# Performance work log

Measured on AMD Instinct MI355X. Metric: run time of the kernel, lower is better.

## Reference

```python
import jax, jax.numpy as jnp
import numpy as np
import math


def setup_inputs() -> dict:
    key = jax.random.key(0)
    ks = jax.random.split(key, 8)
    B, C, H, W = 8, 512, 48, 48
    Cq = C // 8
    s = 0.05
    return {
        "x": jax.random.normal(ks[0], (B, C, H, W), jnp.float32),
        "Wq": jax.random.normal(ks[1], (Cq, C), jnp.float32) * s,
        "bq": jax.random.normal(ks[2], (Cq,), jnp.float32) * s,
        "Wk": jax.random.normal(ks[3], (Cq, C), jnp.float32) * s,
        "bk": jax.random.normal(ks[4], (Cq,), jnp.float32) * s,
        "Wv": jax.random.normal(ks[5], (C, C), jnp.float32) * s,
        "bv": jax.random.normal(ks[6], (C,), jnp.float32) * s,
        "gamma": jax.random.normal(ks[7], (1,), jnp.float32),
    }


def reference(x, Wq, bq, Wk, bk, Wv, bv, gamma):
    B, C, H, W = x.shape
    Cq = Wq.shape[0]
    N = H * W
    xf = x.reshape(B, C, N)  # 1x1 conv == channel matmul
    q = jnp.einsum('oc,bcn->bno', Wq, xf) + bq  # [B, N, Cq] (proj_query, permuted)
    k = jnp.einsum('oc,bcn->bon', Wk, xf) + bk[None, :, None]  # [B, Cq, N]
    v = jnp.einsum('oc,bcn->bon', Wv, xf) + bv[None, :, None]  # [B, C, N]
    # ave_I = (1/Cq)*(I - (1/Cq)*J); Q @ ave_I = (Q - rowmean(Q)) / Cq
    qc = (q - jnp.mean(q, axis=-1, keepdims=True)) / Cq
    sigma = jnp.einsum('bnc,bcm->bnm', qc, k) / math.sqrt(Cq)  # [B, N, N]
    attention = jax.nn.softmax(sigma, axis=-1)
    # out = V @ attention^T : out[b,c,n] = sum_m v[b,c,m] * attention[b,n,m]
    am = jnp.einsum('bcm,bnm->bcn', v, attention).reshape(B, C, H, W)
    out = gamma[0] * am + x
    return out
```

## Files before the change

kernel.cpp:

```cpp
#include <hip/hip_runtime.h>

#define B_ 8
#define C_ 512
#define N_ 2304
#define CQ 64

typedef float f32x2 __attribute__((ext_vector_type(2)));
typedef float f32x4 __attribute__((ext_vector_type(4)));
typedef float f32x16 __attribute__((ext_vector_type(16)));
typedef short bf16x8 __attribute__((ext_vector_type(8)));
typedef unsigned short u16x4 __attribute__((ext_vector_type(4)));
typedef unsigned short u16x8 __attribute__((ext_vector_type(8)));
typedef int i32x2 __attribute__((ext_vector_type(2)));
typedef int i32x4 __attribute__((ext_vector_type(4)));

__device__ __forceinline__ unsigned short f2bf(float f){
  union { float f; unsigned int u; } v; v.f = f;
  unsigned int r = (v.u + 0x7fffu + ((v.u >> 16) & 1u)) >> 16;
  return (unsigned short)r;
}

__device__ __forceinline__ void gload_lds16(const void* g, void* l){
  __builtin_amdgcn_global_load_lds(
      (const __attribute__((address_space(1))) unsigned int*)g,
      (__attribute__((address_space(3))) unsigned int*)l, 16, 0, 0);
}

__global__ __launch_bounds__(256) void k_wcvt(const float* __restrict__ Wq,
                                              const float* __restrict__ Wk,
                                              const float* __restrict__ Wv,
                                              unsigned short* __restrict__ Wb){
  int idx = blockIdx.x*256 + threadIdx.x;
  int h = idx & 1, ln = (idx >> 1) & 31, cs = (idx >> 6) & 31, ob = idx >> 11;
  int row = ob*32 + ln, col = cs*16 + h*8;
  const float* src;
  if (row < 64)       src = Wq + (size_t)row*512 + col;
  else if (row < 128) src = Wk + (size_t)(row-64)*512 + col;
  else                src = Wv + (size_t)(row-128)*512 + col;
  f32x4 v0 = *(const f32x4*)src;
  f32x4 v1 = *(const f32x4*)(src + 4);
  u16x8 o;
  #pragma unroll
  for (int j = 0; j < 4; j++){ o[j] = f2bf(v0[j]); o[4+j] = f2bf(v1[j]); }
  *(u16x8*)(Wb + (size_t)idx*8) = o;
}

__global__ __launch_bounds__(512) void k_prep(const float* __restrict__ x,
                                              const float* __restrict__ bq,
                                              const float* __restrict__ bk,
                                              const float* __restrict__ bv,
                                              const unsigned short* __restrict__ Wb,
                                              unsigned short* __restrict__ qw,
                                              unsigned short* __restrict__ kw,
                                              unsigned char* __restrict__ vw8){
  __shared__ short xt_l[32*520];
  __shared__ float scr[2*32*68];

  int i = blockIdx.x; int b = i & 7; int nt = i >> 3;
  int n0 = nt*32;
  int t = threadIdx.x; int w = t >> 6; int l = t & 63;
  int h = l >> 5, ln = l & 31;
  const size_t bN = (size_t)b*N_;

  #pragma unroll
  for (int it = 0; it < 8; it++){
    int c = it*64 + (t >> 3);
    int n4 = (t & 7)*4;
    f32x4 v = *(const f32x4*)(x + ((size_t)b*C_ + c)*N_ + n0 + n4);
    #pragma unroll
    for (int j = 0; j < 4; j++) xt_l[(n4+j)*520 + c] = (short)f2bf(v[j]);
  }
  __syncthreads();

  const unsigned short* wlane = Wb + (size_t)(ln*2 + h)*8;
  const unsigned short* wv0 = wlane + (size_t)(4 + 2*w)*16384;
  const unsigned short* wv1 = wlane + (size_t)(5 + 2*w)*16384;
  const unsigned short* wqk = wlane + (size_t)w*16384;

  f32x16 vacc[2]; f32x16 qkacc;
  #pragma unroll
  for (int rr = 0; rr < 16; rr++){ vacc[0][rr]=0.f; vacc[1][rr]=0.f; qkacc[rr]=0.f; }

  #pragma unroll 8
  for (int cs = 0; cs < 32; cs++){
    bf16x8 bx = *(const bf16x8*)&xt_l[ln*520 + cs*16 + h*8];
    bf16x8 a0 = *(const bf16x8*)(wv0 + (size_t)cs*512);
    bf16x8 a1 = *(const bf16x8*)(wv1 + (size_t)cs*512);
    vacc[0] = __builtin_amdgcn_mfma_f32_32x32x16_bf16(a0, bx, vacc[0], 0, 0, 0);
    vacc[1] = __builtin_amdgcn_mfma_f32_32x32x16_bf16(a1, bx, vacc[1], 0, 0, 0);
    if (w < 4){
      bf16x8 aq = *(const bf16x8*)(wqk + (size_t)cs*512);
      qkacc = __builtin_amdgcn_mfma_f32_32x32x16_bf16(aq, bx, qkacc, 0, 0, 0);
    }
  }

  if (w < 4){
    float* s = scr + ((w >> 1) ? 2176 : 0);
    int obase = (w & 1)*32;
    #pragma unroll
    for (int rr = 0; rr < 16; rr++){
      int o = obase + (rr & 3) + 8*(rr >> 2) + 4*h;
      s[ln*68 + o] = qkacc[rr];
    }
  }
  __syncthreads();

  if (t < 256){
    int isK = t >> 7;
    int tt = t & 127;
    int n = tt >> 2, j = tt & 3;
    const float* s = scr + (isK ? 2176 : 0);
    const float* bias = isK ? bk : bq;
    float vals[16]; float sm = 0.f;
    #pragma unroll
    for (int ii = 0; ii < 16; ii++){
      vals[ii] = s[n*68 + j*16 + ii] + bias[j*16 + ii];
      sm += vals[ii];
    }
    sm += __shfl_xor(sm, 1); sm += __shfl_xor(sm, 2);
    float mean = isK ? 0.f : sm * (1.f/64.f);
    float scl  = isK ? 1.f : (1.44269504089f/512.f);
    u16x8 h0, h1;
    #pragma unroll
    for (int ii = 0; ii < 8; ii++) h0[ii] = f2bf((vals[ii]   - mean)*scl);
    #pragma unroll
    for (int ii = 0; ii < 8; ii++) h1[ii] = f2bf((vals[8+ii] - mean)*scl);
    unsigned short* d = (isK ? kw : qw) + (bN + n0 + n)*CQ + j*16;
    *(u16x8*)d = h0;
    *(u16x8*)(d + 8) = h1;
  }
  __syncthreads();

  #pragma unroll
  for (int r = 0; r < 4; r++){
    if ((w >> 1) == r){
      float* s = scr + (w & 1)*2176;
      #pragma unroll
      for (int of = 0; of < 2; of++)
        #pragma unroll
        for (int rr = 0; rr < 16; rr++){
          int o = of*32 + (rr & 3) + 8*(rr >> 2) + 4*h;
          s[ln*68 + o] = vacc[of][rr];
        }
    }
    __syncthreads();
    {
      int ch = t >> 8;
      int tt = t & 255;
      int o = tt >> 2, jj = (tt >> 1) & 1, half = tt & 1;
      int og = (2*r + ch)*64 + o;
      const float* s = scr + ch*2176;
      float bvv = bv[og];
      float vv[8];
      #pragma unroll
      for (int ii = 0; ii < 8; ii++){
        int q2 = ((ii & 3) | ((ii & 4) << 1)) + half*4;
        vv[ii] = s[(jj*16 + q2)*68 + o] + bvv;
      }
      int w0 = __builtin_amdgcn_cvt_pk_fp8_f32(vv[0], vv[1], 0,  false);
      w0     = __builtin_amdgcn_cvt_pk_fp8_f32(vv[2], vv[3], w0, true);
      int w1 = __builtin_amdgcn_cvt_pk_fp8_f32(vv[4], vv[5], 0,  false);
      w1     = __builtin_amdgcn_cvt_pk_fp8_f32(vv[6], vv[7], w1, true);
      size_t dst = ((size_t)b*C_ + og)*N_ + n0 + jj*16 + half*8;
      *(i32x2*)(vw8 + dst) = (i32x2){w0, w1};
    }
    __syncthreads();
  }
}

__global__ __launch_bounds__(256) void k_sexp(const unsigned short* __restrict__ qw,
                                              const unsigned short* __restrict__ kw,
                                              unsigned char* __restrict__ Plf,
                                              float* __restrict__ lsum_part,
                                              int b0, int bsh){
  int bid = blockIdx.x;
  int bl = bid & ((1 << bsh) - 1);
  int b = b0 + bl;
  int r = bid >> bsh;
  int ms = r & 3; int nt = r >> 2;
  int t = threadIdx.x; int w = t >> 6; int l = t & 63;
  int h = l >> 5, ln = l & 31;
  int nf = w & 1, mh = w >> 1;
  int n = nt*64 + nf*32 + ln;

  const unsigned short* qb = qw + ((size_t)b*N_ + n)*CQ + h*8;
  bf16x8 qf[4];
  #pragma unroll
  for (int kq = 0; kq < 4; kq++) qf[kq] = *(const bf16x8*)(qb + kq*16);

  int mb32base = ms*18 + mh*9;
  const unsigned short* ks0 = kw + ((size_t)b*N_ + ln)*CQ + h*8 + (size_t)mb32base*32*CQ;
  unsigned char* pbf = Plf + (((size_t)bl*72*N_ + n)*32) + h*16;

  float lsum = 0.f;
  bf16x8 ka[4], kc[4];
  #pragma unroll
  for (int kq = 0; kq < 4; kq++) ka[kq] = *(const bf16x8*)(ks0 + kq*16);

  #define SEXP_BODY(MF, KF, KN, PFOFF)                                          \
  {                                                                             \
    _Pragma("unroll")                                                           \
    for (int kq = 0; kq < 4; kq++)                                              \
      KN[kq] = *(const bf16x8*)(ks0 + (size_t)(PFOFF)*32*CQ + kq*16);           \
    f32x16 sv;                                                                  \
    _Pragma("unroll")                                                           \
    for (int rr = 0; rr < 16; rr++) sv[rr] = 0.f;                               \
    _Pragma("unroll")                                                           \
    for (int kq = 0; kq < 4; kq++)                                              \
      sv = __builtin_amdgcn_mfma_f32_32x32x16_bf16(KF[kq], qf[kq], sv, 0, 0, 0);\
    float e[16];                                                                \
    _Pragma("unroll")                                                           \
    for (int rr = 0; rr < 16; rr++) e[rr] = exp2f(sv[rr]);                      \
    _Pragma("unroll")                                                           \
    for (int rr = 0; rr < 16; rr++) lsum += e[rr];                              \
    int w0 = __builtin_amdgcn_cvt_pk_fp8_f32(e[0],  e[1],  0,  false);          \
    w0     = __builtin_amdgcn_cvt_pk_fp8_f32(e[2],  e[3],  w0, true);           \
    int w1 = __builtin_amdgcn_cvt_pk_fp8_f32(e[4],  e[5],  0,  false);          \
    w1     = __builtin_amdgcn_cvt_pk_fp8_f32(e[6],  e[7],  w1, true);           \
    int w2 = __builtin_amdgcn_cvt_pk_fp8_f32(e[8],  e[9],  0,  false);          \
    w2     = __builtin_amdgcn_cvt_pk_fp8_f32(e[10], e[11], w2, true);           \
    int w3 = __builtin_amdgcn_cvt_pk_fp8_f32(e[12], e[13], 0,  false);          \
    w3     = __builtin_amdgcn_cvt_pk_fp8_f32(e[14], e[15], w3, true);           \
    i32x4 pk4 = (i32x4){w0, w1, w2, w3};                                        \
    *(i32x4*)(pbf + (size_t)(mb32base + (MF))*((size_t)N_*32)) = pk4;           \
  }

  #pragma unroll
  for (int it = 0; it < 4; it++){
    SEXP_BODY(2*it,     ka, kc, 2*it + 1)
    SEXP_BODY(2*it + 1, kc, ka, 2*it + 2)
  }
  SEXP_BODY(8, ka, kc, 8)
  #undef SEXP_BODY

  lsum += __shfl_xor(lsum, 32);
  if (l < 32)
    lsum_part[((size_t)bl*8 + ms*2 + mh)*N_ + n] = lsum;
}

__global__ __launch_bounds__(256, 1) void k_pv(const unsigned char* __restrict__ vw8,
                                               const unsigned char* __restrict__ Plf,
                                               const float* __restrict__ lsum_part,
                                               const float* __restrict__ x,
                                               const float* __restrict__ gamma_p,
                                               float* __restrict__ out,
                                               int b0, int bsh){
  __shared__ __attribute__((aligned(16))) char At[3][8192];

  int bid = blockIdx.x;
  int bl = bid & ((1 << bsh) - 1);
  int b = b0 + bl;
  int r = bid >> bsh;
  int cb = r & 3; int nb = r >> 2;
  int c0 = cb*128, n0g = nb*64;
  int t = threadIdx.x; int w = t >> 6; int l = t & 63;
  int h = l >> 5, ln = l & 31;
  int wc = w & 1, wn = w >> 1;

  const unsigned char* asrc[2];
  int adst[2];
  #pragma unroll
  for (int j = 0; j < 2; j++){
    int row = j*64 + (t >> 2);
    int pos = t & 3;
    int f = (row + (row >> 2)) & 3;
    int q = (pos - f) & 3;
    asrc[j] = vw8 + ((size_t)b*C_ + c0 + row)*N_ + q*16;
    adst[j] = j*4096 + w*1024;
  }
  int aro[2][4];
  #pragma unroll
  for (int cf = 0; cf < 2; cf++)
    #pragma unroll
    for (int mb = 0; mb < 4; mb++){
      int row = wc*64 + cf*32 + ln;
      int f = (row + (row >> 2)) & 3;
      aro[cf][mb] = row*64 + ((mb + f) & 3)*16 + h*8;
    }
  const unsigned char* Pbf = Plf + (size_t)bl*72*N_*32;
  size_t pstep = (size_t)N_*32;
  size_t boffB = (size_t)(n0g + wn*32 + ln)*32 + h*16;

  f32x16 acc[2];
  #pragma unroll
  for (int cf = 0; cf < 2; cf++)
    #pragma unroll
    for (int rr = 0; rr < 16; rr++) acc[cf][rr] = 0.f;

  union bu { i32x4 v; long lg[2]; };
  bu B0[2], B1[2], B2[2];

  #pragma unroll
  for (int j = 0; j < 2; j++)
    gload_lds16(asrc[j], At[0] + adst[j]);
  B0[0].v = *(const i32x4*)(Pbf + boffB);
  B0[1].v = *(const i32x4*)(Pbf + pstep + boffB);
  #pragma unroll
  for (int j = 0; j < 2; j++)
    gload_lds16(asrc[j] + 64, At[1] + adst[j]);
  B1[0].v = *(const i32x4*)(Pbf + 2*pstep + boffB);
  B1[1].v = *(const i32x4*)(Pbf + 3*pstep + boffB);
  asm volatile("s_waitcnt vmcnt(6)" ::: "memory");
  __builtin_amdgcn_s_barrier();
  __builtin_amdgcn_sched_barrier(0);

  #define PV_STEP(KT, RD, WR, BC, BN)                                           \
  {                                                                             \
    const char* Ab = (const char*)At[RD];                                       \
    long a_[2][4];                                                              \
    _Pragma("unroll")                                                           \
    for (int cf = 0; cf < 2; cf++)                                              \
      _Pragma("unroll")                                                         \
      for (int mb = 0; mb < 4; mb++)                                            \
        a_[cf][mb] = *(const long*)(Ab + aro[cf][mb]);                          \
    int m2 = ((KT) + 2 < 36) ? ((KT) + 2)*64 : 0;                               \
    _Pragma("unroll")                                                           \
    for (int j = 0; j < 2; j++)                                                 \
      gload_lds16(asrc[j] + m2, At[WR] + adst[j]);                              \
    {                                                                           \
      size_t pr2 = (size_t)((((KT) + 2 < 36) ? ((KT) + 2)*2 : 0));              \
      BN[0].v = *(const i32x4*)(Pbf + pr2*pstep + boffB);                       \
      BN[1].v = *(const i32x4*)(Pbf + (pr2 + 1)*pstep + boffB);                 \
    }                                                                           \
    _Pragma("unroll")                                                           \
    for (int cf = 0; cf < 2; cf++)                                              \
      _Pragma("unroll")                                                         \
      for (int mb = 0; mb < 4; mb++)                                            \
        acc[cf] = __builtin_amdgcn_mfma_f32_32x32x16_fp8_fp8(                   \
            a_[cf][mb], BC[mb >> 1].lg[mb & 1], acc[cf], 0, 0, 0);              \
    asm volatile("s_waitcnt vmcnt(6) lgkmcnt(0)" ::: "memory");                 \
    __builtin_amdgcn_s_barrier();                                               \
    __builtin_amdgcn_sched_barrier(0);                                          \
  }

  for (int it = 0; it < 6; it++){
    int kt = it*6;
    PV_STEP(kt+0, 0, 2, B0, B2)
    PV_STEP(kt+1, 1, 0, B1, B0)
    PV_STEP(kt+2, 2, 1, B2, B1)
    PV_STEP(kt+3, 0, 2, B0, B2)
    PV_STEP(kt+4, 1, 0, B1, B0)
    PV_STEP(kt+5, 2, 1, B2, B1)
  }
  #undef PV_STEP

  float gmv = gamma_p[0];
  {
    int n = n0g + wn*32 + ln;
    float s = 0.f;
    #pragma unroll
    for (int j = 0; j < 8; j++) s += lsum_part[((size_t)bl*8 + j)*N_ + n];
    float f = gmv / s;
    #pragma unroll
    for (int cf = 0; cf < 2; cf++){
      #pragma unroll
      for (int rr = 0; rr < 16; rr++){
        int c = c0 + wc*64 + cf*32 + (rr & 3) + 8*(rr >> 2) + 4*h;
        size_t idx = ((size_t)b*C_ + c)*N_ + n;
        out[idx] = acc[cf][rr]*f + x[idx];
      }
    }
  }
}

extern "C" void kernel_launch(void* const* d_in, const int* in_sizes, int n_in,
                              void* d_out, int out_size, void* d_ws, size_t ws_size,
                              hipStream_t stream) {
  (void)in_sizes; (void)n_in; (void)out_size;
  const float* x  = (const float*)d_in[0];
  const float* Wq = (const float*)d_in[1];
  const float* bq = (const float*)d_in[2];
  const float* Wk = (const float*)d_in[3];
  const float* bk = (const float*)d_in[4];
  const float* Wv = (const float*)d_in[5];
  const float* bv = (const float*)d_in[6];
  const float* gm = (const float*)d_in[7];
  float* out = (float*)d_out;

  const size_t qw_b = (size_t)B_*N_*CQ*2;
  const size_t vw_b = (size_t)B_*C_*N_;
  const size_t wb_b = (size_t)640*512*2;

  int nbg = 8, bsh = 3;
  for (;;){
    size_t pl_b   = (size_t)nbg*72*N_*32;
    size_t lsum_b = (size_t)nbg*8*N_*4;
    size_t need   = pl_b + 2*qw_b + vw_b + lsum_b + wb_b;
    if (need <= ws_size || nbg == 1) break;
    nbg >>= 1; bsh--;
  }
  size_t pl_b   = (size_t)nbg*72*N_*32;
  size_t lsum_b = (size_t)nbg*8*N_*4;

  char* wsc = (char*)d_ws;
  unsigned char* Plf = (unsigned char*)wsc;
  unsigned short* qw = (unsigned short*)(wsc + pl_b);
  unsigned short* kw = (unsigned short*)(wsc + pl_b + qw_b);
  unsigned char* vw8 = (unsigned char*)(wsc + pl_b + 2*qw_b);
  float* lsum_part   = (float*)(wsc + pl_b + 2*qw_b + vw_b);
  unsigned short* Wb = (unsigned short*)(wsc + pl_b + 2*qw_b + vw_b + lsum_b);

  k_wcvt<<<160, 256, 0, stream>>>(Wq, Wk, Wv, Wb);
  k_prep<<<576, 512, 0, stream>>>(x, bq, bk, bv, Wb, qw, kw, vw8);

  for (int b0 = 0; b0 < B_; b0 += nbg){
    k_sexp<<<144*nbg, 256, 0, stream>>>(qw, kw, Plf, lsum_part, b0, bsh);
    k_pv<<<144*nbg, 256, 0, stream>>>(vw8, Plf, lsum_part, x, gm, out, b0, bsh);
  }
}
```

Before: 110.6 us.

## Double PV k-tile depth and switch LDS A layout to column-slab form

The PV kernel now processes 128 keys per pipeline step instead of 64, halving the number of barrier-synchronised steps, and triple-buffered LDS grows to 48KB. The swizzled row-major A layout is replaced by a slab layout where each 16-byte column chunk of all 128 rows is stored contiguously, removing the XOR-style swizzle arithmetic. This cuts sync overhead per MFMA and allows more loads in flight, at the cost of more registers for operands and prefetched B fragments and more LDS, which may reduce occupancy or cause LDS bank conflicts.

```diff
diff --git a/kernel.cpp b/kernel.cpp
--- a/kernel.cpp
+++ b/kernel.cpp
@@ -245,7 +245,7 @@
                                                const float* __restrict__ gamma_p,
                                                float* __restrict__ out,
                                                int b0, int bsh){
-  __shared__ __attribute__((aligned(16))) char At[3][8192];
+  __shared__ __attribute__((aligned(16))) char At[3][16384];
 
   int bid = blockIdx.x;
   int bl = bid & ((1 << bsh) - 1);
@@ -257,25 +257,21 @@
   int h = l >> 5, ln = l & 31;
   int wc = w & 1, wn = w >> 1;
 
-  const unsigned char* asrc[2];
-  int adst[2];
-  #pragma unroll
-  for (int j = 0; j < 2; j++){
-    int row = j*64 + (t >> 2);
-    int pos = t & 3;
-    int f = (row + (row >> 2)) & 3;
-    int q = (pos - f) & 3;
-    asrc[j] = vw8 + ((size_t)b*C_ + c0 + row)*N_ + q*16;
-    adst[j] = j*4096 + w*1024;
-  }
-  int aro[2][4];
+  const unsigned char* asrc[4];
+  #pragma unroll
+  for (int j = 0; j < 4; j++){
+    int pos = j*2 + (t >> 7);
+    int row = t & 127;
+    asrc[j] = vw8 + ((size_t)b*C_ + c0 + row)*N_ + pos*16;
+  }
+  int adst0 = w*1024 + l*16;
+  int aro[2][8];
   #pragma unroll
   for (int cf = 0; cf < 2; cf++)
     #pragma unroll
-    for (int mb = 0; mb < 4; mb++){
+    for (int mb = 0; mb < 8; mb++){
       int row = wc*64 + cf*32 + ln;
-      int f = (row + (row >> 2)) & 3;
-      aro[cf][mb] = row*64 + ((mb + f) & 3)*16 + h*8;
+      aro[cf][mb] = mb*2048 + row*16 + h*8;
     }
   const unsigned char* Pbf = Plf + (size_t)bl*72*N_*32;
   size_t pstep = (size_t)N_*32;
@@ -288,59 +284,59 @@
     for (int rr = 0; rr < 16; rr++) acc[cf][rr] = 0.f;
 
   union bu { i32x4 v; long lg[2]; };
-  bu B0[2], B1[2], B2[2];
-
-  #pragma unroll
-  for (int j = 0; j < 2; j++)
-    gload_lds16(asrc[j], At[0] + adst[j]);
-  B0[0].v = *(const i32x4*)(Pbf + boffB);
-  B0[1].v = *(const i32x4*)(Pbf + pstep + boffB);
-  #pragma unroll
-  for (int j = 0; j < 2; j++)
-    gload_lds16(asrc[j] + 64, At[1] + adst[j]);
-  B1[0].v = *(const i32x4*)(Pbf + 2*pstep + boffB);
-  B1[1].v = *(const i32x4*)(Pbf + 3*pstep + boffB);
-  asm volatile("s_waitcnt vmcnt(6)" ::: "memory");
+  bu B0[4], B1[4], B2[4];
+
+  #pragma unroll
+  for (int j = 0; j < 4; j++)
+    gload_lds16(asrc[j], At[0] + j*4096 + adst0);
+  #pragma unroll
+  for (int p = 0; p < 4; p++)
+    B0[p].v = *(const i32x4*)(Pbf + (size_t)p*pstep + boffB);
+  #pragma unroll
+  for (int j = 0; j < 4; j++)
+    gload_lds16(asrc[j] + 128, At[1] + j*4096 + adst0);
+  #pragma unroll
+  for (int p = 0; p < 4; p++)
+    B1[p].v = *(const i32x4*)(Pbf + (size_t)(4 + p)*pstep + boffB);
+  asm volatile("s_waitcnt vmcnt(12)" ::: "memory");
   __builtin_amdgcn_s_barrier();
   __builtin_amdgcn_sched_barrier(0);
 
   #define PV_STEP(KT, RD, WR, BC, BN)                                           \
   {                                                                             \
     const char* Ab = (const char*)At[RD];                                       \
-    long a_[2][4];                                                              \
+    long a_[2][8];                                                              \
     _Pragma("unroll")                                                           \
     for (int cf = 0; cf < 2; cf++)                                              \
       _Pragma("unroll")                                                         \
-      for (int mb = 0; mb < 4; mb++)                                            \
+      for (int mb = 0; mb < 8; mb++)                                            \
         a_[cf][mb] = *(const long*)(Ab + aro[cf][mb]);                          \
-    int m2 = ((KT) + 2 < 36) ? ((KT) + 2)*64 : 0;                               \
-    _Pragma("unroll")                                                           \
-    for (int j = 0; j < 2; j++)                                                 \
-      gload_lds16(asrc[j] + m2, At[WR] + adst[j]);                              \
+    int m2 = ((KT) + 2 < 18) ? ((KT) + 2)*128 : 0;                              \
+    _Pragma("unroll")                                                           \
+    for (int j = 0; j < 4; j++)                                                 \
+      gload_lds16(asrc[j] + m2, At[WR] + j*4096 + adst0);                       \
     {                                                                           \
-      size_t pr2 = (size_t)((((KT) + 2 < 36) ? ((KT) + 2)*2 : 0));              \
-      BN[0].v = *(const i32x4*)(Pbf + pr2*pstep + boffB);                       \
-      BN[1].v = *(const i32x4*)(Pbf + (pr2 + 1)*pstep + boffB);                 \
+      size_t pr2 = (size_t)((((KT) + 2 < 18) ? ((KT) + 2)*4 : 0));              \
+      _Pragma("unroll")                                                         \
+      for (int p = 0; p < 4; p++)                                               \
+        BN[p].v = *(const i32x4*)(Pbf + (pr2 + p)*pstep + boffB);               \
     }                                                                           \
     _Pragma("unroll")                                                           \
     for (int cf = 0; cf < 2; cf++)                                              \
       _Pragma("unroll")                                                         \
-      for (int mb = 0; mb < 4; mb++)                                            \
+      for (int mb = 0; mb < 8; mb++)                                            \
         acc[cf] = __builtin_amdgcn_mfma_f32_32x32x16_fp8_fp8(                   \
             a_[cf][mb], BC[mb >> 1].lg[mb & 1], acc[cf], 0, 0, 0);              \
-    asm volatile("s_waitcnt vmcnt(6) lgkmcnt(0)" ::: "memory");                 \
+    asm volatile("s_waitcnt vmcnt(12) lgkmcnt(0)" ::: "memory");                \
     __builtin_amdgcn_s_barrier();                                               \
     __builtin_amdgcn_sched_barrier(0);                                          \
   }
 
   for (int it = 0; it < 6; it++){
-    int kt = it*6;
+    int kt = it*3;
     PV_STEP(kt+0, 0, 2, B0, B2)
     PV_STEP(kt+1, 1, 0, B1, B0)
     PV_STEP(kt+2, 2, 1, B2, B1)
-    PV_STEP(kt+3, 0, 2, B0, B2)
-    PV_STEP(kt+4, 1, 0, B1, B0)
-    PV_STEP(kt+5, 2, 1, B2, B1)
   }
   #undef PV_STEP
 
```

Result: slower. 132.1 us (+19.4%).
